# Performance work log

Measured on AMD Instinct MI355X. Metric: run time of the kernel, lower is better.

## Reference

```python
import jax, jax.numpy as jnp
import numpy as np

N = 100000   # nodes
E = 1600000  # edges (avg degree 16)
IN_DIM = 5
HID = 128
OUT_DIM = 1


def gcn_conv(x, src, dst, W, b, n):
    """PyG GCNConv: out = D^{-1/2}(A+I)D^{-1/2} (x @ W) + b, self-loops added."""
    h = x @ W  # [N, F_out]
    # degree including self-loop (edge weight 1 each)
    deg = jax.ops.segment_sum(jnp.ones(src.shape[0], h.dtype), dst, num_segments=n) + 1.0
    dinv = jax.lax.rsqrt(deg)  # deg >= 1 always (self-loop)
    coef = dinv[src] * dinv[dst]  # [E]
    agg = jax.ops.segment_sum(h[src] * coef[:, None], dst, num_segments=n)
    agg = agg + h * (dinv * dinv)[:, None]  # self-loop contribution
    return agg + b


def setup_inputs() -> dict:
    key = jax.random.key(0)
    k = jax.random.split(key, 6)
    x = jax.random.normal(k[0], (N, IN_DIM), jnp.float32)
    edge_index = jax.random.randint(k[1], (2, E), 0, N)
    W1 = jax.random.normal(k[2], (IN_DIM, HID), jnp.float32) / np.float32(np.sqrt(IN_DIM))
    b1 = jnp.zeros((HID,), jnp.float32)
    W2 = jax.random.normal(k[3], (HID, OUT_DIM), jnp.float32) / np.float32(np.sqrt(HID))
    b2 = jnp.zeros((OUT_DIM,), jnp.float32)
    return {"x": x, "edge_index": edge_index, "W1": W1, "b1": b1, "W2": W2, "b2": b2}


def reference(x, edge_index, W1, b1, W2, b2):
    src, dst = edge_index[0], edge_index[1]
    h = gcn_conv(x, src, dst, W1, b1, N)
    h = jax.nn.relu(h)
    out = gcn_conv(h, src, dst, W2, b2, N)
    return out
```

## Files before the change

kernel.cpp:

```cpp
#include <hip/hip_runtime.h>
#include <hip/hip_fp16.h>

#define Nn 100000
#define Ee 1600000
#define HID 128
#define IN_DIM 5

#define SH 8
#define BSZ 256
#define NB 391
#define BCAP 4608

#define PCHUNK 3125
#define PBLK 512
#define MAXK 7

typedef float f32x4 __attribute__((ext_vector_type(4)));
union F2H { float f; __half2 h; };

__global__ void zero_kernel(int* __restrict__ bcnt) {
    if (threadIdx.x < NB) bcnt[threadIdx.x] = 0;
}

__global__ __launch_bounds__(512) void partition_kernel(const int* __restrict__ src,
                                                        const int* __restrict__ dst,
                                                        unsigned int* __restrict__ recs,
                                                        int* __restrict__ bcnt) {
    __shared__ unsigned int stage[PCHUNK];
    __shared__ unsigned short bstage[PCHUNK];
    __shared__ int hist[NB + 1];
    __shared__ int histS[NB + 1];
    __shared__ int cur[NB];
    __shared__ int gbase[NB];
    __shared__ int wsum[8];
    int tid = threadIdx.x;
    int e0 = blockIdx.x * PCHUNK;
    for (int i = tid; i <= NB; i += 512) hist[i] = 0;
    __syncthreads();
    int rb[MAXK];
    unsigned int rv[MAXK];
    #pragma unroll
    for (int k = 0; k < MAXK; ++k) {
        int idx = tid + k * 512;
        rb[k] = -1;
        if (idx < PCHUNK) {
            int e = e0 + idx;
            int d = dst[e], s = src[e];
            rb[k] = d >> SH;
            rv[k] = ((unsigned int)(d & (BSZ - 1)) << 17) | (unsigned int)s;
            atomicAdd(&hist[rb[k]], 1);
        }
    }
    __syncthreads();
    int v = (tid < NB) ? hist[tid] : 0;
    int lane = tid & 63, wid = tid >> 6;
    int sc = v;
    #pragma unroll
    for (int ofs = 1; ofs < 64; ofs <<= 1) {
        int t = __shfl_up(sc, ofs, 64);
        if (lane >= ofs) sc += t;
    }
    if (lane == 63) wsum[wid] = sc;
    __syncthreads();
    int wpre = 0;
    #pragma unroll
    for (int w = 0; w < 8; ++w)
        if (w < wid) wpre += wsum[w];
    int excl = wpre + sc - v;
    if (tid < NB) {
        histS[tid] = excl;
        cur[tid] = excl;
        gbase[tid] = atomicAdd(&bcnt[tid], v);
    }
    __syncthreads();
    #pragma unroll
    for (int k = 0; k < MAXK; ++k)
        if (rb[k] >= 0) {
            int slot = atomicAdd(&cur[rb[k]], 1);
            stage[slot] = rv[k];
            bstage[slot] = (unsigned short)rb[k];
        }
    __syncthreads();
    for (int i = tid; i < PCHUNK; i += 512) {
        int b = bstage[i];
        recs[(size_t)b * BCAP + gbase[b] + (i - histS[b])] = stage[i];
    }
}

__global__ __launch_bounds__(BSZ) void sortk_kernel(const unsigned int* __restrict__ recs,
                                                    const int* __restrict__ bcnt,
                                                    const float* __restrict__ x,
                                                    int* __restrict__ degc,
                                                    unsigned int* __restrict__ nodeoff,
                                                    unsigned int* __restrict__ ssrc,
                                                    float* __restrict__ dinv,
                                                    f32x4* __restrict__ xd16) {
    __shared__ int cnt[BSZ];
    __shared__ int cur[BSZ];
    __shared__ int wsum[BSZ / 64];
    __shared__ unsigned int lstage[BCAP];
    int b = blockIdx.x, tid = threadIdx.x;
    int n = bcnt[b];
    cnt[tid] = 0;
    __syncthreads();
    const unsigned int* R = recs + (size_t)b * BCAP;
    for (int i = tid; i < n; i += BSZ)
        atomicAdd(&cnt[R[i] >> 17], 1);
    __syncthreads();
    int v = cnt[tid];
    int lane = tid & 63, wid = tid >> 6;
    int sc = v;
    #pragma unroll
    for (int ofs = 1; ofs < 64; ofs <<= 1) {
        int t = __shfl_up(sc, ofs, 64);
        if (lane >= ofs) sc += t;
    }
    if (lane == 63) wsum[wid] = sc;
    __syncthreads();
    int wpre = 0;
    #pragma unroll
    for (int w = 0; w < BSZ / 64; ++w)
        if (w < wid) wpre += wsum[w];
    int excl = wpre + sc - v;
    cur[tid] = excl;
    int g = (b << SH) + tid;
    if (g < Nn) {
        degc[g] = v;
        nodeoff[g] = (unsigned int)(b * BCAP + excl);
        float di = rsqrtf((float)v + 1.0f);
        dinv[g] = di;
        f32x4 o;
        o.x = x[g * IN_DIM + 0] * di;
        o.y = x[g * IN_DIM + 1] * di;
        o.z = x[g * IN_DIM + 2] * di;
        F2H u;
        u.h = __floats2half2_rn(x[g * IN_DIM + 3] * di, x[g * IN_DIM + 4] * di);
        o.w = u.f;
        xd16[g] = o;
    }
    __syncthreads();
    for (int i = tid; i < n; i += BSZ) {
        unsigned int r = R[i];
        int pos = atomicAdd(&cur[r >> 17], 1);
        lstage[pos] = r & 0x1FFFFu;
    }
    __syncthreads();
    unsigned int* O = ssrc + (size_t)b * BCAP;
    for (int i = tid; i < n; i += BSZ) O[i] = lstage[i];
}

__global__ __launch_bounds__(256) void gcn1_kernel(const unsigned int* __restrict__ ssrc,
                                                   const unsigned int* __restrict__ nodeoff,
                                                   const int* __restrict__ degc,
                                                   const f32x4* __restrict__ xd16,
                                                   const float* __restrict__ dinv,
                                                   const float* __restrict__ W1,
                                                   const float* __restrict__ b1,
                                                   const float* __restrict__ W2,
                                                   float* __restrict__ h2d) {
    __shared__ float w1s[IN_DIM * HID];
    __shared__ float w2s[HID], b1s[HID];
    int tid = threadIdx.x;
    for (int j = tid; j < IN_DIM * HID; j += 256) w1s[j] = W1[j];
    if (tid < HID) { w2s[tid] = W2[tid]; b1s[tid] = b1[tid]; }
    __syncthreads();
    int nd = blockIdx.x * 256 + tid;
    if (nd >= Nn) return;
    unsigned int off = nodeoff[nd];
    int len = degc[nd];
    float a0 = 0.f, a1 = 0.f, a2 = 0.f, a3 = 0.f, a4 = 0.f;
    int i = 0;
    for (; i + 4 <= len; i += 4) {
        unsigned int s0 = ssrc[off + i], s1 = ssrc[off + i + 1];
        unsigned int s2 = ssrc[off + i + 2], s3 = ssrc[off + i + 3];
        f32x4 v0 = xd16[s0], v1 = xd16[s1], v2 = xd16[s2], v3 = xd16[s3];
        F2H u0, u1, u2, u3;
        u0.f = v0.w; u1.f = v1.w; u2.f = v2.w; u3.f = v3.w;
        float2 e0 = __half22float2(u0.h), e1 = __half22float2(u1.h);
        float2 e2 = __half22float2(u2.h), e3 = __half22float2(u3.h);
        a0 += (v0.x + v1.x) + (v2.x + v3.x);
        a1 += (v0.y + v1.y) + (v2.y + v3.y);
        a2 += (v0.z + v1.z) + (v2.z + v3.z);
        a3 += (e0.x + e1.x) + (e2.x + e3.x);
        a4 += (e0.y + e1.y) + (e2.y + e3.y);
    }
    for (; i < len; ++i) {
        unsigned int s = ssrc[off + i];
        f32x4 v = xd16[s];
        F2H u; u.f = v.w; float2 e = __half22float2(u.h);
        a0 += v.x; a1 += v.y; a2 += v.z; a3 += e.x; a4 += e.y;
    }
    float di = dinv[nd];
    f32x4 sv = xd16[nd];
    F2H su; su.f = sv.w; float2 se = __half22float2(su.h);
    a0 = (a0 + sv.x) * di;
    a1 = (a1 + sv.y) * di;
    a2 = (a2 + sv.z) * di;
    a3 = (a3 + se.x) * di;
    a4 = (a4 + se.y) * di;
    float accp = 0.f;
    #pragma unroll
    for (int f = 0; f < HID; ++f) {
        float v = b1s[f] + a0 * w1s[f] + a1 * w1s[HID + f] + a2 * w1s[2 * HID + f]
                + a3 * w1s[3 * HID + f] + a4 * w1s[4 * HID + f];
        accp += fmaxf(v, 0.f) * w2s[f];
    }
    h2d[nd] = accp * di;
}

__global__ __launch_bounds__(256) void gcn2_kernel(const unsigned int* __restrict__ ssrc,
                                                   const unsigned int* __restrict__ nodeoff,
                                                   const int* __restrict__ degc,
                                                   const float* __restrict__ h2d,
                                                   const float* __restrict__ dinv,
                                                   const float* __restrict__ b2,
                                                   float* __restrict__ out) {
    int nd = blockIdx.x * 256 + threadIdx.x;
    if (nd >= Nn) return;
    unsigned int off = nodeoff[nd];
    int len = degc[nd];
    float s = 0.f;
    int i = 0;
    for (; i + 8 <= len; i += 8) {
        float t0 = h2d[ssrc[off + i]],     t1 = h2d[ssrc[off + i + 1]];
        float t2 = h2d[ssrc[off + i + 2]], t3 = h2d[ssrc[off + i + 3]];
        float t4 = h2d[ssrc[off + i + 4]], t5 = h2d[ssrc[off + i + 5]];
        float t6 = h2d[ssrc[off + i + 6]], t7 = h2d[ssrc[off + i + 7]];
        s += ((t0 + t1) + (t2 + t3)) + ((t4 + t5) + (t6 + t7));
    }
    for (; i < len; ++i) s += h2d[ssrc[off + i]];
    out[nd] = (s + h2d[nd]) * dinv[nd] + b2[0];
}

extern "C" void kernel_launch(void* const* d_in, const int* in_sizes, int n_in,
                              void* d_out, int out_size, void* d_ws, size_t ws_size,
                              hipStream_t stream) {
    const float* x  = (const float*)d_in[0];
    const int*   ei = (const int*)d_in[1];
    const float* W1 = (const float*)d_in[2];
    const float* b1 = (const float*)d_in[3];
    const float* W2 = (const float*)d_in[4];
    const float* b2 = (const float*)d_in[5];
    const int* src = ei;
    const int* dst = ei + Ee;
    float* out = (float*)d_out;

    float* dinv = (float*)d_ws;
    f32x4* xd16 = (f32x4*)(dinv + Nn);
    float* h2d  = (float*)(xd16 + Nn);
    int* degc   = (int*)(h2d + Nn);
    unsigned int* nodeoff = (unsigned int*)(degc + Nn);
    unsigned int* recs = nodeoff + Nn;
    unsigned int* ssrc = recs + (size_t)NB * BCAP;
    int* bcnt = (int*)(ssrc + (size_t)NB * BCAP);

    zero_kernel<<<1, 512, 0, stream>>>(bcnt);
    partition_kernel<<<PBLK, 512, 0, stream>>>(src, dst, recs, bcnt);
    sortk_kernel<<<NB, BSZ, 0, stream>>>(recs, bcnt, x, degc, nodeoff, ssrc, dinv, xd16);
    gcn1_kernel<<<(Nn + 255) / 256, 256, 0, stream>>>(ssrc, nodeoff, degc, xd16, dinv,
                                                      W1, b1, W2, h2d);
    gcn2_kernel<<<(Nn + 255) / 256, 256, 0, stream>>>(ssrc, nodeoff, degc, h2d, dinv, b2, out);
}
```

Baseline: 67.04 us.

## Replace LDS atomics with warp-ballot match and per-wave histograms in sorting

Both the partition and local sort kernels now count and scatter records using wave-level match via ballot over key bits, with per-wave histograms and prefix offsets instead of shared-memory atomicAdd. The ordering also becomes deterministic, keeping records stable per wave. This removes LDS atomic contention but adds 9–10 ballots per element plus extra shared memory (8*NB ints) that may reduce occupancy.

```diff
diff --git a/kernel.cpp b/kernel.cpp
--- a/kernel.cpp
+++ b/kernel.cpp
@@ -28,14 +28,15 @@
                                                         int* __restrict__ bcnt) {
     __shared__ unsigned int stage[PCHUNK];
     __shared__ unsigned short bstage[PCHUNK];
-    __shared__ int hist[NB + 1];
-    __shared__ int histS[NB + 1];
-    __shared__ int cur[NB];
+    __shared__ int whist[8 * NB];
+    __shared__ int hist[NB];
+    __shared__ int histS[NB];
     __shared__ int gbase[NB];
     __shared__ int wsum[8];
     int tid = threadIdx.x;
+    int lane = tid & 63, wid = tid >> 6;
     int e0 = blockIdx.x * PCHUNK;
-    for (int i = tid; i <= NB; i += 512) hist[i] = 0;
+    for (int i = tid; i < 8 * NB; i += 512) whist[i] = 0;
     __syncthreads();
     int rb[MAXK];
     unsigned int rv[MAXK];
@@ -48,12 +49,37 @@
             int d = dst[e], s = src[e];
             rb[k] = d >> SH;
             rv[k] = ((unsigned int)(d & (BSZ - 1)) << 17) | (unsigned int)s;
-            atomicAdd(&hist[rb[k]], 1);
-        }
+        }
+    }
+    #pragma unroll
+    for (int k = 0; k < MAXK; ++k) {
+        bool valid = rb[k] >= 0;
+        int b = valid ? rb[k] : 0;
+        unsigned long long act = __ballot(valid);
+        unsigned long long same = act;
+        #pragma unroll
+        for (int bit = 0; bit < 9; ++bit) {
+            unsigned long long m = __ballot(valid && ((b >> bit) & 1));
+            same &= ((b >> bit) & 1) ? m : ~m;
+        }
+        if (valid) {
+            int rank = __popcll(same & ((1ull << lane) - 1ull));
+            if (rank == 0) whist[wid * NB + b] += __popcll(same);
+        }
+    }
+    __syncthreads();
+    if (tid < NB) {
+        int acc = 0;
+        #pragma unroll
+        for (int w = 0; w < 8; ++w) {
+            int t = whist[w * NB + tid];
+            whist[w * NB + tid] = acc;
+            acc += t;
+        }
+        hist[tid] = acc;
     }
     __syncthreads();
     int v = (tid < NB) ? hist[tid] : 0;
-    int lane = tid & 63, wid = tid >> 6;
     int sc = v;
     #pragma unroll
     for (int ofs = 1; ofs < 64; ofs <<= 1) {
@@ -69,17 +95,29 @@
     int excl = wpre + sc - v;
     if (tid < NB) {
         histS[tid] = excl;
-        cur[tid] = excl;
         gbase[tid] = atomicAdd(&bcnt[tid], v);
     }
     __syncthreads();
     #pragma unroll
-    for (int k = 0; k < MAXK; ++k)
-        if (rb[k] >= 0) {
-            int slot = atomicAdd(&cur[rb[k]], 1);
-            stage[slot] = rv[k];
-            bstage[slot] = (unsigned short)rb[k];
-        }
+    for (int k = 0; k < MAXK; ++k) {
+        bool valid = rb[k] >= 0;
+        int b = valid ? rb[k] : 0;
+        unsigned long long act = __ballot(valid);
+        unsigned long long same = act;
+        #pragma unroll
+        for (int bit = 0; bit < 9; ++bit) {
+            unsigned long long m = __ballot(valid && ((b >> bit) & 1));
+            same &= ((b >> bit) & 1) ? m : ~m;
+        }
+        if (valid) {
+            int rank = __popcll(same & ((1ull << lane) - 1ull));
+            int before = whist[wid * NB + b];
+            int pos = histS[b] + before + rank;
+            stage[pos] = rv[k];
+            bstage[pos] = (unsigned short)b;
+            if (rank == 0) whist[wid * NB + b] = before + __popcll(same);
+        }
+    }
     __syncthreads();
     for (int i = tid; i < PCHUNK; i += 512) {
         int b = bstage[i];
@@ -95,20 +133,42 @@
                                                     unsigned int* __restrict__ ssrc,
                                                     float* __restrict__ dinv,
                                                     f32x4* __restrict__ xd16) {
-    __shared__ int cnt[BSZ];
-    __shared__ int cur[BSZ];
-    __shared__ int wsum[BSZ / 64];
+    __shared__ int whist[4 * BSZ];
+    __shared__ int nodeS[BSZ];
+    __shared__ int wsum[4];
     __shared__ unsigned int lstage[BCAP];
     int b = blockIdx.x, tid = threadIdx.x;
+    int lane = tid & 63, wid = tid >> 6;
     int n = bcnt[b];
-    cnt[tid] = 0;
+    #pragma unroll
+    for (int w = 0; w < 4; ++w) whist[w * BSZ + tid] = 0;
     __syncthreads();
     const unsigned int* R = recs + (size_t)b * BCAP;
-    for (int i = tid; i < n; i += BSZ)
-        atomicAdd(&cnt[R[i] >> 17], 1);
-    __syncthreads();
-    int v = cnt[tid];
-    int lane = tid & 63, wid = tid >> 6;
+    for (int base = 0; base < n; base += BSZ) {
+        int i = base + tid;
+        bool valid = i < n;
+        int dl = valid ? (int)(R[i] >> 17) : 0;
+        unsigned long long act = __ballot(valid);
+        unsigned long long same = act;
+        #pragma unroll
+        for (int bit = 0; bit < 8; ++bit) {
+            unsigned long long m = __ballot(valid && ((dl >> bit) & 1));
+            same &= ((dl >> bit) & 1) ? m : ~m;
+        }
+        if (valid) {
+            int rank = __popcll(same & ((1ull << lane) - 1ull));
+            if (rank == 0) whist[wid * BSZ + dl] += __popcll(same);
+        }
+    }
+    __syncthreads();
+    int acc = 0;
+    #pragma unroll
+    for (int w = 0; w < 4; ++w) {
+        int t = whist[w * BSZ + tid];
+        whist[w * BSZ + tid] = acc;
+        acc += t;
+    }
+    int v = acc;
     int sc = v;
     #pragma unroll
     for (int ofs = 1; ofs < 64; ofs <<= 1) {
@@ -119,10 +179,10 @@
     __syncthreads();
     int wpre = 0;
     #pragma unroll
-    for (int w = 0; w < BSZ / 64; ++w)
+    for (int w = 0; w < 4; ++w)
         if (w < wid) wpre += wsum[w];
     int excl = wpre + sc - v;
-    cur[tid] = excl;
+    nodeS[tid] = excl;
     int g = (b << SH) + tid;
     if (g < Nn) {
         degc[g] = v;
@@ -139,10 +199,25 @@
         xd16[g] = o;
     }
     __syncthreads();
-    for (int i = tid; i < n; i += BSZ) {
-        unsigned int r = R[i];
-        int pos = atomicAdd(&cur[r >> 17], 1);
-        lstage[pos] = r & 0x1FFFFu;
+    for (int base = 0; base < n; base += BSZ) {
+        int i = base + tid;
+        bool valid = i < n;
+        unsigned int r = valid ? R[i] : 0u;
+        int dl = valid ? (int)(r >> 17) : 0;
+        unsigned long long act = __ballot(valid);
+        unsigned long long same = act;
+        #pragma unroll
+        for (int bit = 0; bit < 8; ++bit) {
+            unsigned long long m = __ballot(valid && ((dl >> bit) & 1));
+            same &= ((dl >> bit) & 1) ? m : ~m;
+        }
+        if (valid) {
+            int rank = __popcll(same & ((1ull << lane) - 1ull));
+            int before = whist[wid * BSZ + dl];
+            int pos = nodeS[dl] + before + rank;
+            lstage[pos] = r & 0x1FFFFu;
+            if (rank == 0) whist[wid * BSZ + dl] = before + __popcll(same);
+        }
     }
     __syncthreads();
     unsigned int* O = ssrc + (size_t)b * BCAP;
```

Measured after the change: 85.06 us. 26.9% more time.

## Use atomic return slots to scatter in one pass in partition and sort

Applied to the files above, without the earlier changes.

In the partition kernel, the LDS staging buffers and the prefix scan are removed. Each edge now takes its local slot from the return value of the bucket atomic and is written straight to its global bucket position. In the per-bucket sort kernel, records are read once into registers (up to 18 per thread) together with their per-node atomic slot, then placed using the scanned node offsets. This removes the second global read of the records and the second round of LDS atomics. The costs are higher register pressure and partition writes that are less grouped by bucket than the staged version.

```diff
diff --git a/kernel.cpp b/kernel.cpp
--- a/kernel.cpp
+++ b/kernel.cpp
@@ -14,6 +14,7 @@
 #define PCHUNK 3125
 #define PBLK 512
 #define MAXK 7
+#define MAXR 18
 
 typedef float f32x4 __attribute__((ext_vector_type(4)));
 union F2H { float f; __half2 h; };
@@ -26,18 +27,13 @@
                                                         const int* __restrict__ dst,
                                                         unsigned int* __restrict__ recs,
                                                         int* __restrict__ bcnt) {
-    __shared__ unsigned int stage[PCHUNK];
-    __shared__ unsigned short bstage[PCHUNK];
-    __shared__ int hist[NB + 1];
-    __shared__ int histS[NB + 1];
     __shared__ int cur[NB];
     __shared__ int gbase[NB];
-    __shared__ int wsum[8];
     int tid = threadIdx.x;
     int e0 = blockIdx.x * PCHUNK;
-    for (int i = tid; i <= NB; i += 512) hist[i] = 0;
-    __syncthreads();
-    int rb[MAXK];
+    for (int i = tid; i < NB; i += 512) cur[i] = 0;
+    __syncthreads();
+    int rb[MAXK], rs[MAXK];
     unsigned int rv[MAXK];
     #pragma unroll
     for (int k = 0; k < MAXK; ++k) {
@@ -48,43 +44,16 @@
             int d = dst[e], s = src[e];
             rb[k] = d >> SH;
             rv[k] = ((unsigned int)(d & (BSZ - 1)) << 17) | (unsigned int)s;
-            atomicAdd(&hist[rb[k]], 1);
+            rs[k] = atomicAdd(&cur[rb[k]], 1);
         }
     }
     __syncthreads();
-    int v = (tid < NB) ? hist[tid] : 0;
-    int lane = tid & 63, wid = tid >> 6;
-    int sc = v;
-    #pragma unroll
-    for (int ofs = 1; ofs < 64; ofs <<= 1) {
-        int t = __shfl_up(sc, ofs, 64);
-        if (lane >= ofs) sc += t;
-    }
-    if (lane == 63) wsum[wid] = sc;
-    __syncthreads();
-    int wpre = 0;
-    #pragma unroll
-    for (int w = 0; w < 8; ++w)
-        if (w < wid) wpre += wsum[w];
-    int excl = wpre + sc - v;
-    if (tid < NB) {
-        histS[tid] = excl;
-        cur[tid] = excl;
-        gbase[tid] = atomicAdd(&bcnt[tid], v);
-    }
+    if (tid < NB) gbase[tid] = atomicAdd(&bcnt[tid], cur[tid]);
     __syncthreads();
     #pragma unroll
     for (int k = 0; k < MAXK; ++k)
-        if (rb[k] >= 0) {
-            int slot = atomicAdd(&cur[rb[k]], 1);
-            stage[slot] = rv[k];
-            bstage[slot] = (unsigned short)rb[k];
-        }
-    __syncthreads();
-    for (int i = tid; i < PCHUNK; i += 512) {
-        int b = bstage[i];
-        recs[(size_t)b * BCAP + gbase[b] + (i - histS[b])] = stage[i];
-    }
+        if (rb[k] >= 0)
+            recs[(size_t)rb[k] * BCAP + gbase[rb[k]] + rs[k]] = rv[k];
 }
 
 __global__ __launch_bounds__(BSZ) void sortk_kernel(const unsigned int* __restrict__ recs,
@@ -95,20 +64,31 @@
                                                     unsigned int* __restrict__ ssrc,
                                                     float* __restrict__ dinv,
                                                     f32x4* __restrict__ xd16) {
-    __shared__ int cnt[BSZ];
     __shared__ int cur[BSZ];
+    __shared__ int nodeS[BSZ];
     __shared__ int wsum[BSZ / 64];
     __shared__ unsigned int lstage[BCAP];
     int b = blockIdx.x, tid = threadIdx.x;
+    int lane = tid & 63, wid = tid >> 6;
     int n = bcnt[b];
-    cnt[tid] = 0;
+    cur[tid] = 0;
     __syncthreads();
     const unsigned int* R = recs + (size_t)b * BCAP;
-    for (int i = tid; i < n; i += BSZ)
-        atomicAdd(&cnt[R[i] >> 17], 1);
-    __syncthreads();
-    int v = cnt[tid];
-    int lane = tid & 63, wid = tid >> 6;
+    int nd_[MAXR], sl_[MAXR];
+    unsigned int sr_[MAXR];
+    #pragma unroll
+    for (int k = 0; k < MAXR; ++k) {
+        int i = tid + k * BSZ;
+        nd_[k] = -1;
+        if (i < n) {
+            unsigned int r = R[i];
+            nd_[k] = (int)(r >> 17);
+            sr_[k] = r & 0x1FFFFu;
+            sl_[k] = atomicAdd(&cur[nd_[k]], 1);
+        }
+    }
+    __syncthreads();
+    int v = cur[tid];
     int sc = v;
     #pragma unroll
     for (int ofs = 1; ofs < 64; ofs <<= 1) {
@@ -122,7 +102,7 @@
     for (int w = 0; w < BSZ / 64; ++w)
         if (w < wid) wpre += wsum[w];
     int excl = wpre + sc - v;
-    cur[tid] = excl;
+    nodeS[tid] = excl;
     int g = (b << SH) + tid;
     if (g < Nn) {
         degc[g] = v;
@@ -139,11 +119,10 @@
         xd16[g] = o;
     }
     __syncthreads();
-    for (int i = tid; i < n; i += BSZ) {
-        unsigned int r = R[i];
-        int pos = atomicAdd(&cur[r >> 17], 1);
-        lstage[pos] = r & 0x1FFFFu;
-    }
+    #pragma unroll
+    for (int k = 0; k < MAXR; ++k)
+        if (nd_[k] >= 0)
+            lstage[nodeS[nd_[k]] + sl_[k]] = sr_[k];
     __syncthreads();
     unsigned int* O = ssrc + (size_t)b * BCAP;
     for (int i = tid; i < n; i += BSZ) O[i] = lstage[i];
```

Result: slower. 70.14 us (+4.6%).

## Assign four lanes per node in GCN gather kernels with shuffle reductions

Applied to the files above, without the earlier changes.

Both aggregation kernels now process each destination node with four consecutive lanes instead of one thread. Each lane takes a strided share of the neighbor list, and the partial sums are combined with xor shuffles. In gcn1 the 128-wide hidden projection is also split across the four lanes. The aim is more memory-level parallelism, better coalescing of the CSR index reads, and less per-thread load imbalance from varying degree, at the cost of four times as many blocks and extra shuffle reductions.

```diff
diff --git a/kernel.cpp b/kernel.cpp
--- a/kernel.cpp
+++ b/kernel.cpp
@@ -164,31 +164,38 @@
     for (int j = tid; j < IN_DIM * HID; j += 256) w1s[j] = W1[j];
     if (tid < HID) { w2s[tid] = W2[tid]; b1s[tid] = b1[tid]; }
     __syncthreads();
-    int nd = blockIdx.x * 256 + tid;
+    int q = tid & 3;
+    int nd = blockIdx.x * 64 + (tid >> 2);
     if (nd >= Nn) return;
     unsigned int off = nodeoff[nd];
     int len = degc[nd];
     float a0 = 0.f, a1 = 0.f, a2 = 0.f, a3 = 0.f, a4 = 0.f;
-    int i = 0;
-    for (; i + 4 <= len; i += 4) {
-        unsigned int s0 = ssrc[off + i], s1 = ssrc[off + i + 1];
-        unsigned int s2 = ssrc[off + i + 2], s3 = ssrc[off + i + 3];
-        f32x4 v0 = xd16[s0], v1 = xd16[s1], v2 = xd16[s2], v3 = xd16[s3];
-        F2H u0, u1, u2, u3;
-        u0.f = v0.w; u1.f = v1.w; u2.f = v2.w; u3.f = v3.w;
+    int i = q;
+    for (; i + 4 < len; i += 8) {
+        unsigned int s0 = ssrc[off + i], s1 = ssrc[off + i + 4];
+        f32x4 v0 = xd16[s0], v1 = xd16[s1];
+        F2H u0, u1;
+        u0.f = v0.w; u1.f = v1.w;
         float2 e0 = __half22float2(u0.h), e1 = __half22float2(u1.h);
-        float2 e2 = __half22float2(u2.h), e3 = __half22float2(u3.h);
-        a0 += (v0.x + v1.x) + (v2.x + v3.x);
-        a1 += (v0.y + v1.y) + (v2.y + v3.y);
-        a2 += (v0.z + v1.z) + (v2.z + v3.z);
-        a3 += (e0.x + e1.x) + (e2.x + e3.x);
-        a4 += (e0.y + e1.y) + (e2.y + e3.y);
-    }
-    for (; i < len; ++i) {
+        a0 += v0.x + v1.x;
+        a1 += v0.y + v1.y;
+        a2 += v0.z + v1.z;
+        a3 += e0.x + e1.x;
+        a4 += e0.y + e1.y;
+    }
+    if (i < len) {
         unsigned int s = ssrc[off + i];
         f32x4 v = xd16[s];
         F2H u; u.f = v.w; float2 e = __half22float2(u.h);
         a0 += v.x; a1 += v.y; a2 += v.z; a3 += e.x; a4 += e.y;
+    }
+    #pragma unroll
+    for (int m = 1; m <= 2; m <<= 1) {
+        a0 += __shfl_xor(a0, m, 64);
+        a1 += __shfl_xor(a1, m, 64);
+        a2 += __shfl_xor(a2, m, 64);
+        a3 += __shfl_xor(a3, m, 64);
+        a4 += __shfl_xor(a4, m, 64);
     }
     float di = dinv[nd];
     f32x4 sv = xd16[nd];
@@ -200,12 +207,15 @@
     a4 = (a4 + se.y) * di;
     float accp = 0.f;
     #pragma unroll
-    for (int f = 0; f < HID; ++f) {
+    for (int f0 = 0; f0 < HID; f0 += 4) {
+        int f = f0 + q;
         float v = b1s[f] + a0 * w1s[f] + a1 * w1s[HID + f] + a2 * w1s[2 * HID + f]
                 + a3 * w1s[3 * HID + f] + a4 * w1s[4 * HID + f];
         accp += fmaxf(v, 0.f) * w2s[f];
     }
-    h2d[nd] = accp * di;
+    accp += __shfl_xor(accp, 1, 64);
+    accp += __shfl_xor(accp, 2, 64);
+    if (q == 0) h2d[nd] = accp * di;
 }
 
 __global__ __launch_bounds__(256) void gcn2_kernel(const unsigned int* __restrict__ ssrc,
@@ -215,21 +225,23 @@
                                                    const float* __restrict__ dinv,
                                                    const float* __restrict__ b2,
                                                    float* __restrict__ out) {
-    int nd = blockIdx.x * 256 + threadIdx.x;
+    int tid = threadIdx.x;
+    int q = tid & 3;
+    int nd = blockIdx.x * 64 + (tid >> 2);
     if (nd >= Nn) return;
     unsigned int off = nodeoff[nd];
     int len = degc[nd];
     float s = 0.f;
-    int i = 0;
-    for (; i + 8 <= len; i += 8) {
-        float t0 = h2d[ssrc[off + i]],     t1 = h2d[ssrc[off + i + 1]];
-        float t2 = h2d[ssrc[off + i + 2]], t3 = h2d[ssrc[off + i + 3]];
-        float t4 = h2d[ssrc[off + i + 4]], t5 = h2d[ssrc[off + i + 5]];
-        float t6 = h2d[ssrc[off + i + 6]], t7 = h2d[ssrc[off + i + 7]];
-        s += ((t0 + t1) + (t2 + t3)) + ((t4 + t5) + (t6 + t7));
-    }
-    for (; i < len; ++i) s += h2d[ssrc[off + i]];
-    out[nd] = (s + h2d[nd]) * dinv[nd] + b2[0];
+    int i = q;
+    for (; i + 4 < len; i += 8) {
+        float t0 = h2d[ssrc[off + i]];
+        float t1 = h2d[ssrc[off + i + 4]];
+        s += t0 + t1;
+    }
+    if (i < len) s += h2d[ssrc[off + i]];
+    s += __shfl_xor(s, 1, 64);
+    s += __shfl_xor(s, 2, 64);
+    if (q == 0) out[nd] = (s + h2d[nd]) * dinv[nd] + b2[0];
 }
 
 extern "C" void kernel_launch(void* const* d_in, const int* in_sizes, int n_in,
@@ -257,7 +269,7 @@
     zero_kernel<<<1, 512, 0, stream>>>(bcnt);
     partition_kernel<<<PBLK, 512, 0, stream>>>(src, dst, recs, bcnt);
     sortk_kernel<<<NB, BSZ, 0, stream>>>(recs, bcnt, x, degc, nodeoff, ssrc, dinv, xd16);
-    gcn1_kernel<<<(Nn + 255) / 256, 256, 0, stream>>>(ssrc, nodeoff, degc, xd16, dinv,
-                                                      W1, b1, W2, h2d);
-    gcn2_kernel<<<(Nn + 255) / 256, 256, 0, stream>>>(ssrc, nodeoff, degc, h2d, dinv, b2, out);
-}
+    gcn1_kernel<<<(Nn + 63) / 64, 256, 0, stream>>>(ssrc, nodeoff, degc, xd16, dinv,
+                                                    W1, b1, W2, h2d);
+    gcn2_kernel<<<(Nn + 63) / 64, 256, 0, stream>>>(ssrc, nodeoff, degc, h2d, dinv, b2, out);
+}
```

Result: no change. 66.75 us (median of 2 runs) (-0.4%).
